# Kernel optimization log

Measured on AMD Instinct MI355X. Metric: run time of the kernel, lower is better.

The kernel has to match this reference:

```python
import jax, jax.numpy as jnp
import numpy as np

L, D, F, H, K, V, E = 15, 512, 2048, 64, 128, 30, 1024
DH = D // H  # 8
B, N = 8, 128


def _ln(x, s, b, eps=1e-5):
    m = x.mean(-1, keepdims=True)
    v = ((x - m) ** 2).mean(-1, keepdims=True)
    return (x - m) * jax.lax.rsqrt(v + eps) * s + b


def _gauss(x, mean, std):
    # matches torch.jit gaussian(): pi = 3.14159
    a = (2.0 * 3.14159) ** 0.5
    return jnp.exp(-0.5 * ((x - mean) / std) ** 2) / (a * std)


def setup_inputs() -> dict:
    key = jax.random.key(0)
    ks = iter(jax.random.split(key, 48))
    nrm = lambda shape, sc=0.02: jax.random.normal(next(ks), shape, jnp.float32) * sc
    zeros = lambda shape: jnp.zeros(shape, jnp.float32)
    ones = lambda shape: jnp.ones(shape, jnp.float32)
    return dict(
        src_tokens=jax.random.randint(next(ks), (B, N), 0, V),
        src_distance=jax.random.uniform(next(ks), (B, N, N), jnp.float32) * 3.0,
        src_edge_type=jax.random.randint(next(ks), (B, N, N), 0, E),
        token_embed=nrm((V, D)),
        gbf_means=jax.random.uniform(next(ks), (K,), jnp.float32, 0.0, 3.0),
        gbf_stds=jax.random.uniform(next(ks), (K,), jnp.float32, 0.0, 3.0),
        gbf_mul=ones((E, 1)),
        gbf_bias=zeros((E, 1)),
        proj_w1=nrm((K, K)), proj_b1=zeros((K,)),
        proj_w2=nrm((K, H)), proj_b2=zeros((H,)),
        emb_ln_s=ones((D,)), emb_ln_b=zeros((D,)),
        Wq=nrm((L, D, D)), bq=zeros((L, D)),
        Wk=nrm((L, D, D)), bk=zeros((L, D)),
        Wv=nrm((L, D, D)), bv=zeros((L, D)),
        Wo=nrm((L, D, D)), bo=zeros((L, D)),
        ln1_s=ones((L, D)), ln1_b=zeros((L, D)),
        ln2_s=ones((L, D)), ln2_b=zeros((L, D)),
        Wf1=nrm((L, D, F)), bf1=zeros((L, F)),
        Wf2=nrm((L, F, D)), bf2=zeros((L, D)),
        fin_ln_s=ones((D,)), fin_ln_b=zeros((D,)),
    )


def reference(src_tokens, src_distance, src_edge_type, token_embed,
              gbf_means, gbf_stds, gbf_mul, gbf_bias,
              proj_w1, proj_b1, proj_w2, proj_b2,
              emb_ln_s, emb_ln_b,
              Wq, bq, Wk, bk, Wv, bv, Wo, bo,
              ln1_s, ln1_b, ln2_s, ln2_b,
              Wf1, bf1, Wf2, bf2, fin_ln_s, fin_ln_b):
    # --- GaussianLayer: per-pair edge-type affine + K-kernel RBF -> [B,N,N,K]
    mul = gbf_mul[src_edge_type]          # [B,N,N,1]
    add = gbf_bias[src_edge_type]         # [B,N,N,1]
    g = mul * src_distance[..., None] + add
    std = jnp.abs(gbf_stds) + 1e-5
    g = _gauss(g, gbf_means, std)         # broadcast [B,N,N,1] vs [K] -> [B,N,N,K]
    # --- gbf_proj (NonLinearHead K->K->H) -> attention bias [B,H,N,N]
    hproj = jax.nn.gelu(g @ proj_w1 + proj_b1, approximate=False)
    bias0 = jnp.transpose(hproj @ proj_w2 + proj_b2, (0, 3, 1, 2))

    x = _ln(token_embed[src_tokens], emb_ln_s, emb_ln_b)  # [B,N,D]
    scale = DH ** -0.5

    def layer(carry, p):
        x, bias = carry
        wq, bq_, wk, bk_, wv, bv_, wo, bo_, s1, b1, s2, b2, wf1, bf1_, wf2, bf2_ = p
        # pre-LN self-attention with additive pair bias
        r = x
        y = _ln(x, s1, b1)
        q = (y @ wq + bq_).reshape(B, N, H, DH) * scale
        k = (y @ wk + bk_).reshape(B, N, H, DH)
        v = (y @ wv + bv_).reshape(B, N, H, DH)
        scores = jnp.einsum('bihd,bjhd->bhij', q, k) + bias  # [B,H,N,N]
        probs = jax.nn.softmax(scores, axis=-1)
        o = jnp.einsum('bhij,bjhd->bihd', probs, v).reshape(B, N, D)
        x = r + (o @ wo + bo_)
        # pre-LN FFN
        r = x
        y = _ln(x, s2, b2)
        y = jax.nn.gelu(y @ wf1 + bf1_, approximate=False) @ wf2 + bf2_
        # UniMol: pre-softmax scores feed the next layer as its pair bias
        return (r + y, scores), None

    (x, _), _ = jax.lax.scan(
        layer, (x, bias0),
        (Wq, bq, Wk, bk, Wv, bv, Wo, bo, ln1_s, ln1_b, ln2_s, ln2_b, Wf1, bf1, Wf2, bf2))
    return _ln(x, fin_ln_s, fin_ln_b)  # [B,N,D]
```

## Files before the change

### kernel.cpp

```cpp
#include <hip/hip_runtime.h>
#include <hip/hip_bf16.h>

#define Bv 8
#define Nv 128
#define Dv 512
#define Hv 64
#define DHv 8
#define Fv 2048
#define Lv 15
#define Kv 128

typedef unsigned short u16;
typedef __attribute__((ext_vector_type(8))) short s16x8;
typedef __attribute__((ext_vector_type(4))) float f32x4;

__device__ __forceinline__ float b2f(u16 u) {
    union { unsigned int i; float f; } w;
    w.i = ((unsigned int)u) << 16;
    return w.f;
}

__device__ __forceinline__ u16 f2b(float f) {
    __hip_bfloat16 h = __float2bfloat16(f);
    u16 u;
    __builtin_memcpy(&u, &h, 2);
    return u;
}

__device__ __forceinline__ bool probe_bf16(const void* p) {
    return ((const u16*)p)[0] == 0x3F80u;
}

__device__ __forceinline__ float ldv(const u16* p, size_t i)   { return b2f(p[i]); }
__device__ __forceinline__ float ldv(const float* p, size_t i) { return p[i]; }

__device__ __forceinline__ u16 ld16(const u16* p, size_t i)   { return p[i]; }
__device__ __forceinline__ u16 ld16(const float* p, size_t i) { return f2b(p[i]); }

__device__ __forceinline__ float geluf(float v) {
    return 0.5f * v * (1.0f + erff(v * 0.70710678118654752f));
}

template<typename T>
__device__ __forceinline__ void gbf2_body(
    const T* dist, const int* etype, const T* means, const T* stds,
    const T* mulW, const T* addW, const T* w1, const T* b1w,
    const T* w2, const T* b2w, float* biasOut,
    float* xs, float* smean, float* sinv, u16* GA, u16* Bst)
{
    const int t = threadIdx.x;
    const int iq = blockIdx.x;
    const int j0 = blockIdx.y << 6;
    const int b = blockIdx.z;

    if (t < 64) {
        size_t pidx = ((size_t)(b * Nv + iq)) * Nv + j0 + t;
        int e = etype[pidx];
        xs[t] = ldv(dist, pidx) * ldv(mulW, e) + ldv(addW, e);
    } else if (t >= 128) {
        int k = t - 128;
        float sv = fabsf(ldv(stds, k)) + 1e-5f;
        smean[k] = ldv(means, k);
        sinv[k] = 1.0f / sv;
    }
    __syncthreads();

    {
        const int row = t & 63;
        const int kc = t >> 6;
        const float x = xs[row];
        const int mt = row >> 4, r = row & 15;
        #pragma unroll
        for (int lg2 = 0; lg2 < 4; lg2++) {
            union { s16x8 v; u16 u[8]; } pk;
            #pragma unroll
            for (int j = 0; j < 8; j++) {
                int k = kc * 32 + lg2 * 8 + j;
                float z = (x - smean[k]) * sinv[k];
                pk.u[j] = f2b(expf(-0.5f * z * z) * (0.39894261f * sinv[k]));
            }
            *reinterpret_cast<s16x8*>(&GA[(((mt * 4 + kc) * 4 + lg2) * 16 + r) << 3]) = pk.v;
        }
    }

    const int w = t >> 6, l = t & 63;
    const int lg = l >> 4, lr = l & 15;
    const int wm = (w >> 1) << 5;
    const int wn1 = (w & 1) << 6;
    const int mt0 = wm >> 4;

    const int b1col = t & 127, b1lg0 = (t >> 7) << 1;

    f32x4 acc1[2][4];
    #pragma unroll
    for (int mi = 0; mi < 2; mi++)
        #pragma unroll
        for (int ni = 0; ni < 4; ni++) acc1[mi][ni] = (f32x4){0.f, 0.f, 0.f, 0.f};

    for (int kc = 0; kc < 4; kc++) {
        #pragma unroll
        for (int q = 0; q < 2; q++) {
            int lgq = b1lg0 + q;
            union { s16x8 v; u16 u[8]; } pb;
            #pragma unroll
            for (int j = 0; j < 8; j++)
                pb.u[j] = ld16(w1, (size_t)(kc * 32 + lgq * 8 + j) * Kv + b1col);
            *reinterpret_cast<s16x8*>(
                &Bst[((((b1col >> 4) * 4 + lgq) * 16 + (b1col & 15)) << 3)]) = pb.v;
        }
        __syncthreads();
        s16x8 a0 = *reinterpret_cast<const s16x8*>(&GA[((((mt0 + 0) * 4 + kc) * 4 + lg) * 16 + lr) << 3]);
        s16x8 a1 = *reinterpret_cast<const s16x8*>(&GA[((((mt0 + 1) * 4 + kc) * 4 + lg) * 16 + lr) << 3]);
        #pragma unroll
        for (int ni = 0; ni < 4; ni++) {
            int nt = (wn1 >> 4) + ni;
            s16x8 bf = *reinterpret_cast<const s16x8*>(&Bst[((nt * 4 + lg) * 16 + lr) << 3]);
            acc1[0][ni] = __builtin_amdgcn_mfma_f32_16x16x32_bf16(a0, bf, acc1[0][ni], 0, 0, 0);
            acc1[1][ni] = __builtin_amdgcn_mfma_f32_16x16x32_bf16(a1, bf, acc1[1][ni], 0, 0, 0);
        }
        __syncthreads();
    }

    #pragma unroll
    for (int mi = 0; mi < 2; mi++) {
        #pragma unroll
        for (int ni = 0; ni < 4; ni++) {
            int col = wn1 + ni * 16 + lr;
            float bb = ldv(b1w, col);
            #pragma unroll
            for (int i = 0; i < 4; i++) {
                int row = wm + mi * 16 + lg * 4 + i;
                float v = geluf(acc1[mi][ni][i] + bb);
                GA[((((row >> 4) * 4 + (col >> 5)) * 4 + ((col >> 3) & 3)) * 16 + (row & 15)) * 8 + (col & 7)] = f2b(v);
            }
        }
    }
    __syncthreads();

    const int wn2 = (w & 1) << 5;
    const int b2col = t & 63, b2lg = t >> 6;

    f32x4 acc2[2][2];
    #pragma unroll
    for (int mi = 0; mi < 2; mi++)
        #pragma unroll
        for (int ni = 0; ni < 2; ni++) acc2[mi][ni] = (f32x4){0.f, 0.f, 0.f, 0.f};

    for (int kc = 0; kc < 4; kc++) {
        {
            union { s16x8 v; u16 u[8]; } pb;
            #pragma unroll
            for (int j = 0; j < 8; j++)
                pb.u[j] = ld16(w2, (size_t)(kc * 32 + b2lg * 8 + j) * Hv + b2col);
            *reinterpret_cast<s16x8*>(
                &Bst[((((b2col >> 4) * 4 + b2lg) * 16 + (b2col & 15)) << 3)]) = pb.v;
        }
        __syncthreads();
        s16x8 a0 = *reinterpret_cast<const s16x8*>(&GA[((((mt0 + 0) * 4 + kc) * 4 + lg) * 16 + lr) << 3]);
        s16x8 a1 = *reinterpret_cast<const s16x8*>(&GA[((((mt0 + 1) * 4 + kc) * 4 + lg) * 16 + lr) << 3]);
        #pragma unroll
        for (int ni = 0; ni < 2; ni++) {
            int nt = (wn2 >> 4) + ni;
            s16x8 bf = *reinterpret_cast<const s16x8*>(&Bst[((nt * 4 + lg) * 16 + lr) << 3]);
            acc2[0][ni] = __builtin_amdgcn_mfma_f32_16x16x32_bf16(a0, bf, acc2[0][ni], 0, 0, 0);
            acc2[1][ni] = __builtin_amdgcn_mfma_f32_16x16x32_bf16(a1, bf, acc2[1][ni], 0, 0, 0);
        }
        __syncthreads();
    }

    #pragma unroll
    for (int mi = 0; mi < 2; mi++) {
        #pragma unroll
        for (int ni = 0; ni < 2; ni++) {
            int h = wn2 + ni * 16 + lr;
            int jb = wm + mi * 16 + lg * 4;
            float badd = ldv(b2w, h);
            size_t oidx = (((size_t)(b * Hv + h)) * Nv + iq) * Nv + j0 + jb;
            *reinterpret_cast<float4*>(&biasOut[oidx]) =
                make_float4(acc2[mi][ni][0] + badd, acc2[mi][ni][1] + badd,
                            acc2[mi][ni][2] + badd, acc2[mi][ni][3] + badd);
        }
    }
}

__global__ __launch_bounds__(256) void gbf2_k(
    const void* dist, const int* etype, const void* means, const void* stds,
    const void* mulW, const void* addW, const void* w1, const void* b1,
    const void* w2, const void* b2, float* biasOut, const void* probe)
{
    __shared__ float xs[64];
    __shared__ float smean[Kv];
    __shared__ float sinv[Kv];
    __shared__ __align__(16) u16 GA[8192];
    __shared__ __align__(16) u16 Bst[4096];
    if (probe_bf16(probe))
        gbf2_body<u16>((const u16*)dist, etype, (const u16*)means, (const u16*)stds,
                       (const u16*)mulW, (const u16*)addW, (const u16*)w1, (const u16*)b1,
                       (const u16*)w2, (const u16*)b2, biasOut, xs, smean, sinv, GA, Bst);
    else
        gbf2_body<float>((const float*)dist, etype, (const float*)means, (const float*)stds,
                         (const float*)mulW, (const float*)addW, (const float*)w1, (const float*)b1,
                         (const float*)w2, (const float*)b2, biasOut, xs, smean, sinv, GA, Bst);
}

__device__ __forceinline__ void block_stats_512(float x0, float x1, float& mean, float& rstd)
{
    float sum = x0 + x1, sq = x0 * x0 + x1 * x1;
    #pragma unroll
    for (int off = 32; off; off >>= 1) {
        sum += __shfl_xor(sum, off);
        sq  += __shfl_xor(sq, off);
    }
    __shared__ float ssum[4], ssq[4];
    int t = threadIdx.x;
    if ((t & 63) == 0) { ssum[t >> 6] = sum; ssq[t >> 6] = sq; }
    __syncthreads();
    sum = ssum[0] + ssum[1] + ssum[2] + ssum[3];
    sq  = ssq[0] + ssq[1] + ssq[2] + ssq[3];
    mean = sum * (1.0f / 512.0f);
    float var = sq * (1.0f / 512.0f) - mean * mean;
    rstd = rsqrtf(var + 1e-5f);
}

template<typename T>
__device__ __forceinline__ void embed_body(
    const int* toks, const T* emb, const T* sc, const T* bi, float* xout)
{
    int row = blockIdx.x, t = threadIdx.x;
    int tok = toks[row];
    float x0 = ldv(emb, (size_t)tok * Dv + t);
    float x1 = ldv(emb, (size_t)tok * Dv + t + 256);
    float mean, rstd;
    block_stats_512(x0, x1, mean, rstd);
    xout[(size_t)row * Dv + t]       = (x0 - mean) * rstd * ldv(sc, t) + ldv(bi, t);
    xout[(size_t)row * Dv + t + 256] = (x1 - mean) * rstd * ldv(sc, t + 256) + ldv(bi, t + 256);
}

__global__ __launch_bounds__(256) void embed_ln_k(
    const int* toks, const void* emb, const void* sc, const void* bi,
    float* xout, const void* probe)
{
    if (probe_bf16(probe))
        embed_body<u16>(toks, (const u16*)emb, (const u16*)sc, (const u16*)bi, xout);
    else
        embed_body<float>(toks, (const float*)emb, (const float*)sc, (const float*)bi, xout);
}

template<typename T>
__device__ __forceinline__ void ln_body(
    const float* xin, const T* sc, const T* bi, size_t pofs, u16* yout)
{
    int row = blockIdx.x, t = threadIdx.x;
    const float* xp = xin + (size_t)row * Dv;
    float x0 = xp[t], x1 = xp[t + 256];
    float mean, rstd;
    block_stats_512(x0, x1, mean, rstd);
    yout[(size_t)row * Dv + t]       = f2b((x0 - mean) * rstd * ldv(sc, pofs + t) + ldv(bi, pofs + t));
    yout[(size_t)row * Dv + t + 256] = f2b((x1 - mean) * rstd * ldv(sc, pofs + t + 256) + ldv(bi, pofs + t + 256));
}

__global__ __launch_bounds__(256) void ln_k(
    const float* xin, const void* sc, const void* bi, unsigned long long pofs,
    u16* yout, const void* probe)
{
    if (probe_bf16(probe))
        ln_body<u16>(xin, (const u16*)sc, (const u16*)bi, (size_t)pofs, yout);
    else
        ln_body<float>(xin, (const float*)sc, (const float*)bi, (size_t)pofs, yout);
}

template<typename T, bool OUT_BF>
__device__ __forceinline__ void final_ln_body(
    const float* xin, const T* sc, const T* bi, void* yout)
{
    int row = blockIdx.x, t = threadIdx.x;
    const float* xp = xin + (size_t)row * Dv;
    float x0 = xp[t], x1 = xp[t + 256];
    float mean, rstd;
    block_stats_512(x0, x1, mean, rstd);
    float o0 = (x0 - mean) * rstd * ldv(sc, t) + ldv(bi, t);
    float o1 = (x1 - mean) * rstd * ldv(sc, t + 256) + ldv(bi, t + 256);
    if (OUT_BF) {
        __hip_bfloat16* yp = (__hip_bfloat16*)yout;
        yp[(size_t)row * Dv + t]       = __float2bfloat16(o0);
        yp[(size_t)row * Dv + t + 256] = __float2bfloat16(o1);
    } else {
        float* yp = (float*)yout;
        yp[(size_t)row * Dv + t]       = o0;
        yp[(size_t)row * Dv + t + 256] = o1;
    }
}

__global__ __launch_bounds__(256) void final_ln_k(
    const float* xin, const void* sc, const void* bi, void* yout, const void* probe)
{
    if (probe_bf16(probe))
        final_ln_body<u16, true>(xin, (const u16*)sc, (const u16*)bi, yout);
    else
        final_ln_body<float, false>(xin, (const float*)sc, (const float*)bi, yout);
}

template<typename T>
__device__ __forceinline__ void gemm_mfma_body(
    const u16* A, const T* W, const T* bias, const float* R,
    void* C, int Nc, int Kc, int act, int res, int kbegin, int kend,
    int raw, int cbf, u16* Al, u16* Bl)
{
    const int tid = threadIdx.x;
    const int l = tid & 63, w = tid >> 6;
    const int wm = (w >> 1) << 5, wn = (w & 1) << 5;
    const int bm = blockIdx.y * 64, bn = blockIdx.x * 64;
    const int lg = l >> 4, lr = l & 15;
    const int mt0 = wm >> 4, nt0 = wn >> 4;

    f32x4 acc00 = {}, acc01 = {}, acc10 = {}, acc11 = {};

    const int arow = tid >> 2, akq = tid & 3;
    const u16* aGp = A + (size_t)(bm + arow) * Kc + (akq << 3);
    const int aL0 = ((((arow >> 4) * 2 + 0) * 4 + akq) * 16 + (arow & 15)) << 3;
    const int aL1 = ((((arow >> 4) * 2 + 1) * 4 + akq) * 16 + (arow & 15)) << 3;

    const int bcol = tid & 63;
    const int be = tid >> 6;
    const int bc = be >> 1, blg0 = (be & 1) << 1;
    const int bnt = bcol >> 4, bcl = bcol & 15;
    const int bL0 = (((bnt * 2 + bc) * 4 + blg0) * 16 + bcl) << 3;
    const int bL1 = (((bnt * 2 + bc) * 4 + blg0 + 1) * 16 + bcl) << 3;

    s16x8 ra0, ra1, rb0, rb1;
    ra0 = *reinterpret_cast<const s16x8*>(aGp + kbegin);
    ra1 = *reinterpret_cast<const s16x8*>(aGp + kbegin + 32);
    {
        union { s16x8 v; u16 u[8]; } p0, p1;
        #pragma unroll
        for (int j = 0; j < 8; j++) {
            p0.u[j] = ld16(W, (size_t)(kbegin + bc * 32 + blg0 * 8 + j) * Nc + bn + bcol);
            p1.u[j] = ld16(W, (size_t)(kbegin + bc * 32 + blg0 * 8 + 8 + j) * Nc + bn + bcol);
        }
        rb0 = p0.v; rb1 = p1.v;
    }

    for (int kt = kbegin; kt < kend; kt += 64) {
        *reinterpret_cast<s16x8*>(&Al[aL0]) = ra0;
        *reinterpret_cast<s16x8*>(&Al[aL1]) = ra1;
        *reinterpret_cast<s16x8*>(&Bl[bL0]) = rb0;
        *reinterpret_cast<s16x8*>(&Bl[bL1]) = rb1;
        __syncthreads();

        const int kn = kt + 64;
        if (kn < kend) {
            ra0 = *reinterpret_cast<const s16x8*>(aGp + kn);
            ra1 = *reinterpret_cast<const s16x8*>(aGp + kn + 32);
            union { s16x8 v; u16 u[8]; } p0, p1;
            #pragma unroll
            for (int j = 0; j < 8; j++) {
                p0.u[j] = ld16(W, (size_t)(kn + bc * 32 + blg0 * 8 + j) * Nc + bn + bcol);
                p1.u[j] = ld16(W, (size_t)(kn + bc * 32 + blg0 * 8 + 8 + j) * Nc + bn + bcol);
            }
            rb0 = p0.v; rb1 = p1.v;
        }

        #pragma unroll
        for (int c = 0; c < 2; c++) {
            s16x8 af0 = *reinterpret_cast<const s16x8*>(&Al[((((mt0 + 0) * 2 + c) * 4 + lg) * 16 + lr) << 3]);
            s16x8 af1 = *reinterpret_cast<const s16x8*>(&Al[((((mt0 + 1) * 2 + c) * 4 + lg) * 16 + lr) << 3]);
            s16x8 bf0 = *reinterpret_cast<const s16x8*>(&Bl[((((nt0 + 0) * 2 + c) * 4 + lg) * 16 + lr) << 3]);
            s16x8 bf1 = *reinterpret_cast<const s16x8*>(&Bl[((((nt0 + 1) * 2 + c) * 4 + lg) * 16 + lr) << 3]);
            acc00 = __builtin_amdgcn_mfma_f32_16x16x32_bf16(af0, bf0, acc00, 0, 0, 0);
            acc01 = __builtin_amdgcn_mfma_f32_16x16x32_bf16(af0, bf1, acc01, 0, 0, 0);
            acc10 = __builtin_amdgcn_mfma_f32_16x16x32_bf16(af1, bf0, acc10, 0, 0, 0);
            acc11 = __builtin_amdgcn_mfma_f32_16x16x32_bf16(af1, bf1, acc11, 0, 0, 0);
        }
        __syncthreads();
    }

    #pragma unroll
    for (int mi = 0; mi < 2; mi++) {
        #pragma unroll
        for (int i = 0; i < 4; i++) {
            const int row = bm + wm + mi * 16 + lg * 4 + i;
            const float* Rrow = res ? (R + (size_t)row * Nc) : nullptr;
            #pragma unroll
            for (int ni = 0; ni < 2; ni++) {
                const int col = bn + wn + ni * 16 + lr;
                float cv = (ni == 0) ? (mi == 0 ? acc00[i] : acc10[i])
                                     : (mi == 0 ? acc01[i] : acc11[i]);
                if (raw) {
                    ((float*)C)[(size_t)row * Nc + col] = cv;
                } else {
                    cv += ldv(bias, col);
                    if (act) cv = geluf(cv);
                    if (res) cv += Rrow[col];
                    if (cbf) ((u16*)C)[(size_t)row * Nc + col] = f2b(cv);
                    else     ((float*)C)[(size_t)row * Nc + col] = cv;
                }
            }
        }
    }
}

__global__ __launch_bounds__(256) void gemm_k(
    const u16* A, const void* W, unsigned long long wofs,
    const void* bias, unsigned long long bofs, const float* R,
    void* C, int Nc, int Kc, int act, int res, int cbf, const void* probe)
{
    __shared__ __align__(16) u16 Al[4096];
    __shared__ __align__(16) u16 Bl[4096];
    const int nz = gridDim.z, z = blockIdx.z;
    const int kchunk = Kc / nz;
    const int kbegin = z * kchunk, kend = kbegin + kchunk;
    const int raw = (nz > 1) ? 1 : 0;
    void* Cz = (char*)C + (size_t)z * ((size_t)gridDim.y * 64) * Nc * sizeof(float);
    if (probe_bf16(probe))
        gemm_mfma_body<u16>(A, (const u16*)W + wofs, (const u16*)bias + bofs, R, Cz,
                            Nc, Kc, act, res, kbegin, kend, raw, cbf, Al, Bl);
    else
        gemm_mfma_body<float>(A, (const float*)W + wofs, (const float*)bias + bofs, R, Cz,
                              Nc, Kc, act, res, kbegin, kend, raw, cbf, Al, Bl);
}

__global__ __launch_bounds__(256) void qkv_k(
    const u16* A,
    const void* W0, const void* W1p, const void* W2p, unsigned long long wofs,
    const void* b0, const void* b1p, const void* b2p, unsigned long long bofs,
    float* C0, float* C1, float* C2, const void* probe)
{
    __shared__ __align__(16) u16 Al[4096];
    __shared__ __align__(16) u16 Bl[4096];
    const int z = blockIdx.z;
    const void* W  = (z == 0) ? W0 : (z == 1) ? W1p : W2p;
    const void* bb = (z == 0) ? b0 : (z == 1) ? b1p : b2p;
    float* C       = (z == 0) ? C0 : (z == 1) ? C1 : C2;
    if (probe_bf16(probe))
        gemm_mfma_body<u16>(A, (const u16*)W + wofs, (const u16*)bb + bofs, nullptr, C,
                            Dv, Dv, 0, 0, 0, Dv, 0, 0, Al, Bl);
    else
        gemm_mfma_body<float>(A, (const float*)W + wofs, (const float*)bb + bofs, nullptr, C,
                              Dv, Dv, 0, 0, 0, Dv, 0, 0, Al, Bl);
}

template<typename T>
__device__ __forceinline__ void combln_body(
    const float* parts, const T* pbias, float* X,
    const T* lnS, const T* lnB, size_t pofs, u16* Y)
{
    const int t = threadIdx.x;
    const int rowb = t >> 7;
    const int col = (t & 127) << 2;
    const int row = (blockIdx.x << 1) + rowb;
    const size_t idx = (size_t)row * Dv + col;

    float4 sv = *reinterpret_cast<const float4*>(&parts[idx]);
    #pragma unroll
    for (int p = 1; p < 4; p++) {
        const float4 q2 = *reinterpret_cast<const float4*>(&parts[(size_t)p * 524288 + idx]);
        sv.x += q2.x; sv.y += q2.y; sv.z += q2.z; sv.w += q2.w;
    }
    sv.x += ldv(pbias, col);     sv.y += ldv(pbias, col + 1);
    sv.z += ldv(pbias, col + 2); sv.w += ldv(pbias, col + 3);
    const float4 r = *reinterpret_cast<const float4*>(&X[idx]);
    sv.x += r.x; sv.y += r.y; sv.z += r.z; sv.w += r.w;
    *reinterpret_cast<float4*>(&X[idx]) = sv;

    float sum = sv.x + sv.y + sv.z + sv.w;
    float sq  = sv.x * sv.x + sv.y * sv.y + sv.z * sv.z + sv.w * sv.w;
    #pragma unroll
    for (int off = 32; off; off >>= 1) {
        sum += __shfl_xor(sum, off);
        sq  += __shfl_xor(sq, off);
    }
    __shared__ float ssum[4], ssq[4];
    const int wv = t >> 6;
    if ((t & 63) == 0) { ssum[wv] = sum; ssq[wv] = sq; }
    __syncthreads();
    sum = ssum[rowb * 2] + ssum[rowb * 2 + 1];
    sq  = ssq[rowb * 2] + ssq[rowb * 2 + 1];
    const float mean = sum * (1.0f / 512.0f);
    const float var = sq * (1.0f / 512.0f) - mean * mean;
    const float rstd = rsqrtf(var + 1e-5f);

    ushort4 yv;
    yv.x = f2b((sv.x - mean) * rstd * ldv(lnS, pofs + col)     + ldv(lnB, pofs + col));
    yv.y = f2b((sv.y - mean) * rstd * ldv(lnS, pofs + col + 1) + ldv(lnB, pofs + col + 1));
    yv.z = f2b((sv.z - mean) * rstd * ldv(lnS, pofs + col + 2) + ldv(lnB, pofs + col + 2));
    yv.w = f2b((sv.w - mean) * rstd * ldv(lnS, pofs + col + 3) + ldv(lnB, pofs + col + 3));
    *reinterpret_cast<ushort4*>(&Y[idx]) = yv;
}

__global__ __launch_bounds__(256) void combln_k(
    const float* parts, const void* pbias, unsigned long long bofs, float* X,
    const void* lnS, const void* lnB, unsigned long long pofs, u16* Y,
    const void* probe)
{
    if (probe_bf16(probe))
        combln_body<u16>(parts, (const u16*)pbias + bofs, X,
                         (const u16*)lnS, (const u16*)lnB, (size_t)pofs, Y);
    else
        combln_body<float>(parts, (const float*)pbias + bofs, X,
                           (const float*)lnS, (const float*)lnB, (size_t)pofs, Y);
}

__global__ __launch_bounds__(512) void attn_k(
    const float* __restrict__ q, const float* __restrict__ k, const float* __restrict__ v,
    float* bias, u16* __restrict__ o)
{
    __shared__ __align__(16) float ks[Nv][DHv];
    __shared__ __align__(16) float vs[Nv][DHv];

    const int t = threadIdx.x;
    const int h = blockIdx.x;
    const int b = blockIdx.y;
    const int i = (blockIdx.z << 6) + (t >> 3);
    const int e = t & 7;
    const float scale = 0.35355339059327373f;

    const float* kh = k + (size_t)(b * Nv) * Dv + h * DHv;
    const float* vh = v + (size_t)(b * Nv) * Dv + h * DHv;

    {
        const int j = t >> 2, c = (t & 3) << 1;
        const float2 k2 = *reinterpret_cast<const float2*>(kh + (size_t)j * Dv + c);
        const float2 v2 = *reinterpret_cast<const float2*>(vh + (size_t)j * Dv + c);
        *reinterpret_cast<float2*>(&ks[j][c]) = k2;
        *reinterpret_cast<float2*>(&vs[j][c]) = v2;
    }

    const float* qp = q + (size_t)(b * Nv + i) * Dv + h * DHv;
    const float4 q0 = *reinterpret_cast<const float4*>(qp);
    const float4 q1 = *reinterpret_cast<const float4*>(qp + 4);

    float* bp = bias + (((size_t)(b * Hv + h)) * Nv + i) * Nv;

    float s[16];
    #pragma unroll
    for (int w = 0; w < 16; w++) s[w] = bp[(w << 3) + e];

    __syncthreads();

    float mx = -1e30f;
    #pragma unroll
    for (int w = 0; w < 16; w++) {
        const int j = (w << 3) + e;
        const float4 k0 = *reinterpret_cast<const float4*>(&ks[j][0]);
        const float4 k1 = *reinterpret_cast<const float4*>(&ks[j][4]);
        float d = q0.x * k0.x + q0.y * k0.y + q0.z * k0.z + q0.w * k0.w +
                  q1.x * k1.x + q1.y * k1.y + q1.z * k1.z + q1.w * k1.w;
        float val = s[w] + scale * d;
        s[w] = val;
        bp[j] = val;
        mx = fmaxf(mx, val);
    }

    mx = fmaxf(mx, __shfl_xor(mx, 1));
    mx = fmaxf(mx, __shfl_xor(mx, 2));
    mx = fmaxf(mx, __shfl_xor(mx, 4));

    float sum = 0.0f;
    #pragma unroll
    for (int w = 0; w < 16; w++) {
        s[w] = expf(s[w] - mx);
        sum += s[w];
    }
    sum += __shfl_xor(sum, 1);
    sum += __shfl_xor(sum, 2);
    sum += __shfl_xor(sum, 4);
    const float inv = 1.0f / sum;

    float a0 = 0, a1 = 0, a2 = 0, a3 = 0, a4 = 0, a5 = 0, a6 = 0, a7 = 0;
    #pragma unroll
    for (int w = 0; w < 16; w++) {
        const int j = (w << 3) + e;
        const float4 v0 = *reinterpret_cast<const float4*>(&vs[j][0]);
        const float4 v1 = *reinterpret_cast<const float4*>(&vs[j][4]);
        const float p = s[w];
        a0 += p * v0.x; a1 += p * v0.y; a2 += p * v0.z; a3 += p * v0.w;
        a4 += p * v1.x; a5 += p * v1.y; a6 += p * v1.z; a7 += p * v1.w;
    }
    a0 += __shfl_xor(a0, 1); a0 += __shfl_xor(a0, 2); a0 += __shfl_xor(a0, 4);
    a1 += __shfl_xor(a1, 1); a1 += __shfl_xor(a1, 2); a1 += __shfl_xor(a1, 4);
    a2 += __shfl_xor(a2, 1); a2 += __shfl_xor(a2, 2); a2 += __shfl_xor(a2, 4);
    a3 += __shfl_xor(a3, 1); a3 += __shfl_xor(a3, 2); a3 += __shfl_xor(a3, 4);
    a4 += __shfl_xor(a4, 1); a4 += __shfl_xor(a4, 2); a4 += __shfl_xor(a4, 4);
    a5 += __shfl_xor(a5, 1); a5 += __shfl_xor(a5, 2); a5 += __shfl_xor(a5, 4);
    a6 += __shfl_xor(a6, 1); a6 += __shfl_xor(a6, 2); a6 += __shfl_xor(a6, 4);
    a7 += __shfl_xor(a7, 1); a7 += __shfl_xor(a7, 2); a7 += __shfl_xor(a7, 4);

    if (e == 0) {
        u16* op = o + (size_t)(b * Nv + i) * Dv + h * DHv;
        ushort4 o0 = { f2b(a0 * inv), f2b(a1 * inv), f2b(a2 * inv), f2b(a3 * inv) };
        ushort4 o1 = { f2b(a4 * inv), f2b(a5 * inv), f2b(a6 * inv), f2b(a7 * inv) };
        *reinterpret_cast<ushort4*>(op)     = o0;
        *reinterpret_cast<ushort4*>(op + 4) = o1;
    }
}

extern "C" void kernel_launch(void* const* d_in, const int* in_sizes, int n_in,
                              void* d_out, int out_size, void* d_ws, size_t ws_size,
                              hipStream_t stream)
{
    const int*  src_tokens = (const int*)d_in[0];
    const void* src_dist   = d_in[1];
    const int*  src_edge   = (const int*)d_in[2];
    const void* token_emb  = d_in[3];
    const void* gbf_means  = d_in[4];
    const void* gbf_stds   = d_in[5];
    const void* gbf_mul    = d_in[6];
    const void* gbf_bias   = d_in[7];
    const void* pw1        = d_in[8];
    const void* pb1        = d_in[9];
    const void* pw2        = d_in[10];
    const void* pb2        = d_in[11];
    const void* embs       = d_in[12];
    const void* embb       = d_in[13];
    const void* Wq         = d_in[14];
    const void* bq         = d_in[15];
    const void* Wk         = d_in[16];
    const void* bk         = d_in[17];
    const void* Wv         = d_in[18];
    const void* bvp        = d_in[19];
    const void* Wo         = d_in[20];
    const void* bo         = d_in[21];
    const void* ln1s       = d_in[22];
    const void* ln1b       = d_in[23];
    const void* ln2s       = d_in[24];
    const void* ln2b       = d_in[25];
    const void* Wf1        = d_in[26];
    const void* bf1        = d_in[27];
    const void* Wf2        = d_in[28];
    const void* bf2        = d_in[29];
    const void* fins       = d_in[30];
    const void* finb       = d_in[31];
    const void* probe      = embs;

    float* ws   = (float*)d_ws;
    float* x    = ws;
    float* y    = x  + 524288;
    float* qb   = y  + 524288;
    float* kb   = qb + 524288;
    float* vb   = kb + 524288;
    float* ob   = vb + 524288;
    float* hb   = ob + 524288;
    u16*   hbf  = (u16*)hb;
    u16*   ybf  = (u16*)(hb + 1048576);
    u16*   obf  = (u16*)(hb + 1310720);
    float* bias = hb + 2097152;

    gbf2_k<<<dim3(Nv, 2, Bv), 256, 0, stream>>>(
        src_dist, src_edge, gbf_means, gbf_stds, gbf_mul, gbf_bias,
        pw1, pb1, pw2, pb2, bias, probe);
    embed_ln_k<<<Bv * Nv, 256, 0, stream>>>(src_tokens, token_emb, embs, embb, x, probe);
    ln_k<<<Bv * Nv, 256, 0, stream>>>(x, ln1s, ln1b, 0ull, ybf, probe);

    dim3 gQKV(512 / 64, 1024 / 64, 3);
    dim3 gS4(512 / 64, 1024 / 64, 4);
    dim3 gF1(2048 / 64, 1024 / 64);
    for (int l = 0; l < Lv; l++) {
        unsigned long long wofs  = (unsigned long long)l * Dv * Dv;
        unsigned long long wofsF = (unsigned long long)l * Dv * Fv;
        unsigned long long dof   = (unsigned long long)l * Dv;
        unsigned long long fof   = (unsigned long long)l * Fv;
        unsigned long long nofs  = (l + 1 < Lv) ? (unsigned long long)(l + 1) * Dv : 0ull;

        qkv_k<<<gQKV, 256, 0, stream>>>(ybf, Wq, Wk, Wv, wofs, bq, bk, bvp, dof,
                                        qb, kb, vb, probe);
        attn_k<<<dim3(Hv, Bv, 2), 512, 0, stream>>>(qb, kb, vb, bias, obf);
        gemm_k<<<gS4, 256, 0, stream>>>(obf, Wo, wofs, bo, dof, nullptr, y, 512, 512, 0, 0, 0, probe);
        combln_k<<<512, 256, 0, stream>>>(y, bo, dof, x, ln2s, ln2b, dof, ybf, probe);
        gemm_k<<<gF1, 256, 0, stream>>>(ybf, Wf1, wofsF, bf1, fof, nullptr, hbf, 2048, 512, 1, 0, 1, probe);
        gemm_k<<<gS4, 256, 0, stream>>>(hbf, Wf2, wofsF, bf2, fof, nullptr, y, 512, 2048, 0, 0, 0, probe);
        combln_k<<<512, 256, 0, stream>>>(y, bf2, dof, x, ln1s, ln1b, nofs, ybf, probe);
    }
    final_ln_k<<<Bv * Nv, 256, 0, stream>>>(x, fins, finb, d_out, probe);
}
```

Before: 1.471 ms.

## Prefetch GBF projection weights into registers and use fast exp/erf approximations

The gaussian-bias projection kernel now loads the next K-chunk of W1/W2 into registers while the current chunk's MFMAs run. It also issues the first weight loads before the RBF computation so their latency overlaps that work. Separately, expf is replaced by __expf in the RBF and the attention softmax, and erff in GELU is replaced by an Abramowitz-Stegun polynomial approximation. Together these aim to hide global load latency and cut transcendental cost, at the price of slightly lower numerical accuracy and higher register pressure.

```diff
diff --git a/kernel.cpp b/kernel.cpp
--- a/kernel.cpp
+++ b/kernel.cpp
@@ -37,8 +37,17 @@
 __device__ __forceinline__ u16 ld16(const u16* p, size_t i)   { return p[i]; }
 __device__ __forceinline__ u16 ld16(const float* p, size_t i) { return f2b(p[i]); }
 
+__device__ __forceinline__ float erf_fast(float x) {
+    float ax = fabsf(x);
+    float tt = 1.0f / fmaf(0.3275911f, ax, 1.0f);
+    float y = tt * fmaf(tt, fmaf(tt, fmaf(tt, fmaf(tt, 1.061405429f, -1.453152027f),
+                                          1.421413741f), -0.284496736f), 0.254829592f);
+    float r = 1.0f - y * __expf(-ax * ax);
+    return copysignf(r, x);
+}
+
 __device__ __forceinline__ float geluf(float v) {
-    return 0.5f * v * (1.0f + erff(v * 0.70710678118654752f));
+    return 0.5f * v * (1.0f + erf_fast(v * 0.70710678118654752f));
 }
 
 template<typename T>
@@ -65,6 +74,25 @@
     }
     __syncthreads();
 
+    const int w = t >> 6, l = t & 63;
+    const int lg = l >> 4, lr = l & 15;
+    const int wm = (w >> 1) << 5;
+    const int wn1 = (w & 1) << 6;
+    const int mt0 = wm >> 4;
+
+    const int b1col = t & 127, b1lg0 = (t >> 7) << 1;
+
+    s16x8 rb0, rb1;
+    {
+        union { s16x8 v; u16 u[8]; } p0, p1;
+        #pragma unroll
+        for (int j = 0; j < 8; j++) {
+            p0.u[j] = ld16(w1, (size_t)((b1lg0 + 0) * 8 + j) * Kv + b1col);
+            p1.u[j] = ld16(w1, (size_t)((b1lg0 + 1) * 8 + j) * Kv + b1col);
+        }
+        rb0 = p0.v; rb1 = p1.v;
+    }
+
     {
         const int row = t & 63;
         const int kc = t >> 6;
@@ -77,19 +105,12 @@
             for (int j = 0; j < 8; j++) {
                 int k = kc * 32 + lg2 * 8 + j;
                 float z = (x - smean[k]) * sinv[k];
-                pk.u[j] = f2b(expf(-0.5f * z * z) * (0.39894261f * sinv[k]));
+                pk.u[j] = f2b(__expf(-0.5f * z * z) * (0.39894261f * sinv[k]));
             }
             *reinterpret_cast<s16x8*>(&GA[(((mt * 4 + kc) * 4 + lg2) * 16 + r) << 3]) = pk.v;
         }
     }
-
-    const int w = t >> 6, l = t & 63;
-    const int lg = l >> 4, lr = l & 15;
-    const int wm = (w >> 1) << 5;
-    const int wn1 = (w & 1) << 6;
-    const int mt0 = wm >> 4;
-
-    const int b1col = t & 127, b1lg0 = (t >> 7) << 1;
+    __syncthreads();
 
     f32x4 acc1[2][4];
     #pragma unroll
@@ -98,17 +119,22 @@
         for (int ni = 0; ni < 4; ni++) acc1[mi][ni] = (f32x4){0.f, 0.f, 0.f, 0.f};
 
     for (int kc = 0; kc < 4; kc++) {
-        #pragma unroll
-        for (int q = 0; q < 2; q++) {
-            int lgq = b1lg0 + q;
-            union { s16x8 v; u16 u[8]; } pb;
+        *reinterpret_cast<s16x8*>(
+            &Bst[((((b1col >> 4) * 4 + b1lg0 + 0) * 16 + (b1col & 15)) << 3)]) = rb0;
+        *reinterpret_cast<s16x8*>(
+            &Bst[((((b1col >> 4) * 4 + b1lg0 + 1) * 16 + (b1col & 15)) << 3)]) = rb1;
+        __syncthreads();
+
+        if (kc < 3) {
+            union { s16x8 v; u16 u[8]; } p0, p1;
             #pragma unroll
-            for (int j = 0; j < 8; j++)
-                pb.u[j] = ld16(w1, (size_t)(kc * 32 + lgq * 8 + j) * Kv + b1col);
-            *reinterpret_cast<s16x8*>(
-                &Bst[((((b1col >> 4) * 4 + lgq) * 16 + (b1col & 15)) << 3)]) = pb.v;
-        }
-        __syncthreads();
+            for (int j = 0; j < 8; j++) {
+                p0.u[j] = ld16(w1, (size_t)((kc + 1) * 32 + (b1lg0 + 0) * 8 + j) * Kv + b1col);
+                p1.u[j] = ld16(w1, (size_t)((kc + 1) * 32 + (b1lg0 + 1) * 8 + j) * Kv + b1col);
+            }
+            rb0 = p0.v; rb1 = p1.v;
+        }
+
         s16x8 a0 = *reinterpret_cast<const s16x8*>(&GA[((((mt0 + 0) * 4 + kc) * 4 + lg) * 16 + lr) << 3]);
         s16x8 a1 = *reinterpret_cast<const s16x8*>(&GA[((((mt0 + 1) * 4 + kc) * 4 + lg) * 16 + lr) << 3]);
         #pragma unroll
@@ -119,6 +145,16 @@
             acc1[1][ni] = __builtin_amdgcn_mfma_f32_16x16x32_bf16(a1, bf, acc1[1][ni], 0, 0, 0);
         }
         __syncthreads();
+    }
+
+    const int b2col = t & 63, b2lg = t >> 6;
+    s16x8 rc;
+    {
+        union { s16x8 v; u16 u[8]; } pb;
+        #pragma unroll
+        for (int j = 0; j < 8; j++)
+            pb.u[j] = ld16(w2, (size_t)(b2lg * 8 + j) * Hv + b2col);
+        rc = pb.v;
     }
 
     #pragma unroll
@@ -138,7 +174,6 @@
     __syncthreads();
 
     const int wn2 = (w & 1) << 5;
-    const int b2col = t & 63, b2lg = t >> 6;
 
     f32x4 acc2[2][2];
     #pragma unroll
@@ -147,15 +182,18 @@
         for (int ni = 0; ni < 2; ni++) acc2[mi][ni] = (f32x4){0.f, 0.f, 0.f, 0.f};
 
     for (int kc = 0; kc < 4; kc++) {
-        {
+        *reinterpret_cast<s16x8*>(
+            &Bst[((((b2col >> 4) * 4 + b2lg) * 16 + (b2col & 15)) << 3)]) = rc;
+        __syncthreads();
+
+        if (kc < 3) {
             union { s16x8 v; u16 u[8]; } pb;
             #pragma unroll
             for (int j = 0; j < 8; j++)
-                pb.u[j] = ld16(w2, (size_t)(kc * 32 + b2lg * 8 + j) * Hv + b2col);
-            *reinterpret_cast<s16x8*>(
-                &Bst[((((b2col >> 4) * 4 + b2lg) * 16 + (b2col & 15)) << 3)]) = pb.v;
-        }
-        __syncthreads();
+                pb.u[j] = ld16(w2, (size_t)((kc + 1) * 32 + b2lg * 8 + j) * Hv + b2col);
+            rc = pb.v;
+        }
+
         s16x8 a0 = *reinterpret_cast<const s16x8*>(&GA[((((mt0 + 0) * 4 + kc) * 4 + lg) * 16 + lr) << 3]);
         s16x8 a1 = *reinterpret_cast<const s16x8*>(&GA[((((mt0 + 1) * 4 + kc) * 4 + lg) * 16 + lr) << 3]);
         #pragma unroll
@@ -558,7 +596,7 @@
     float sum = 0.0f;
     #pragma unroll
     for (int w = 0; w < 16; w++) {
-        s[w] = expf(s[w] - mx);
+        s[w] = __expf(s[w] - mx);
         sum += s[w];
     }
     sum += __shfl_xor(sum, 1);
```

New measurement: 1.460 ms. About the same (-0.8%).
